# Kernel tuning notes

Measured on AMD Instinct MI355X. Metric: run time of the kernel, lower is better.

Reference implementation:

```python
import jax, jax.numpy as jnp
import numpy as np

N, E, G, F = 50000, 800000, 128, 64  # nodes, edges, graphs, feature dim
EPS = 1e-5


def setup_inputs() -> dict:
    key = jax.random.key(0)
    ks = jax.random.split(key, 16)
    w = lambda k, s: jax.random.normal(k, s, jnp.float32) * 0.05
    inp = {
        "x": jax.random.normal(ks[0], (N, F), jnp.float32),
        # SAGEConv l: lin_l (aggregated neighbors, with bias), lin_r (root, no bias)
        "c0_Wl": w(ks[1], (F, F)), "c0_bl": jnp.zeros((F,), jnp.float32), "c0_Wr": w(ks[2], (F, F)),
        "c1_Wl": w(ks[3], (F, F)), "c1_bl": jnp.zeros((F,), jnp.float32), "c1_Wr": w(ks[4], (F, F)),
        "c2_Wl": w(ks[5], (F, F)), "c2_bl": jnp.zeros((F,), jnp.float32), "c2_Wr": w(ks[6], (F, F)),
        # skip linears (bias=False)
        "s0_W": w(ks[7], (F, F)), "s1_W": w(ks[8], (F, F)),
        # graph-mode LayerNorm affine params
        "ln0_w": jnp.ones((F,), jnp.float32), "ln0_b": jnp.zeros((F,), jnp.float32),
        "ln1_w": jnp.ones((F,), jnp.float32), "ln1_b": jnp.zeros((F,), jnp.float32),
        "ln2_w": jnp.ones((F,), jnp.float32), "ln2_b": jnp.zeros((F,), jnp.float32),
        # PReLU(1): single shared slope, torch default init 0.25
        "p0_a": jnp.full((1,), 0.25, jnp.float32),
        "p1_a": jnp.full((1,), 0.25, jnp.float32),
        "p2_a": jnp.full((1,), 0.25, jnp.float32),
        "edge_index": jax.random.randint(ks[9], (2, E), 0, N, jnp.int64),
        "batch": jnp.sort(jax.random.randint(ks[10], (N,), 0, G, jnp.int64)),
    }
    return inp


def _sage(x, Wl, bl, Wr, src, dst):
    # mean-aggregate source features at destinations, then two linears
    agg = jax.ops.segment_sum(x[src], dst, num_segments=N)            # [N, F]
    deg = jax.ops.segment_sum(jnp.ones((E,), x.dtype), dst, num_segments=N)
    agg = agg / jnp.maximum(deg, 1.0)[:, None]
    return agg @ Wl + bl + x @ Wr


def _graph_ln(x, batch, w, b):
    # PyG LayerNorm mode='graph': normalize over all nodes & channels per graph
    f = x.shape[-1]
    cnt = jax.ops.segment_sum(jnp.ones((x.shape[0],), x.dtype), batch, num_segments=G)
    norm = jnp.maximum(cnt, 1.0) * f                                  # [G]
    mean = jax.ops.segment_sum(x, batch, num_segments=G).sum(-1) / norm
    xc = x - mean[batch][:, None]
    var = jax.ops.segment_sum(xc * xc, batch, num_segments=G).sum(-1) / norm
    out = xc / jnp.sqrt(var + EPS)[batch][:, None]
    return out * w + b


def _prelu(x, a):
    return jnp.where(x >= 0, x, a[0] * x)


def reference(x, c0_Wl, c0_bl, c0_Wr, c1_Wl, c1_bl, c1_Wr, c2_Wl, c2_bl, c2_Wr,
              s0_W, s1_W, ln0_w, ln0_b, ln1_w, ln1_b, ln2_w, ln2_b,
              p0_a, p1_a, p2_a, edge_index, batch):
    src, dst = edge_index[0], edge_index[1]
    h1 = _prelu(_graph_ln(_sage(x, c0_Wl, c0_bl, c0_Wr, src, dst), batch, ln0_w, ln0_b), p0_a)
    h2 = _sage(h1 + x @ s0_W, c1_Wl, c1_bl, c1_Wr, src, dst)
    h2 = _prelu(_graph_ln(h2, batch, ln1_w, ln1_b), p1_a)
    ret = _sage(h1 + h2 + x @ s1_W, c2_Wl, c2_bl, c2_Wr, src, dst)
    ret = _prelu(_graph_ln(ret, batch, ln2_w, ln2_b), p2_a)
    return ret
```

## Files before the change

kernel.cpp:

```cpp
#include <hip/hip_runtime.h>

#define NN 50000
#define NE 800000
#define NG 128
#define NF 64
#define EPSV 1e-5f
#define GB3 782
#define NBUCK 196
#define BCAP 5120

typedef unsigned short ushortT;

__device__ inline unsigned short f2bf(float f) {
  unsigned u = __float_as_uint(f);
  u += 0x7FFF + ((u >> 16) & 1);
  return (unsigned short)(u >> 16);
}
__device__ inline float bflo(unsigned v) { return __uint_as_float(v << 16); }
__device__ inline float bfhi(unsigned v) { return __uint_as_float(v & 0xFFFF0000u); }

__global__ void k_bz(const int* __restrict__ batch, int* __restrict__ bound,
                     int* __restrict__ gcursor, float* __restrict__ stats) {
  int i = blockIdx.x * 256 + threadIdx.x;
  if (blockIdx.x == 0) {
    int t = threadIdx.x;
    if (t < NBUCK) gcursor[t] = 0;
    for (int k = t; k < 6 * NG; k += 256) stats[k] = 0.f;
  }
  if (i >= NN) return;
  int b1 = batch[i];
  int b0 = (i == 0) ? -1 : batch[i - 1];
  for (int g = b0 + 1; g <= b1; ++g) bound[g] = i;
  if (i == NN - 1) {
    for (int g = b1 + 1; g <= NG; ++g) bound[g] = NN;
  }
}

__global__ __launch_bounds__(256) void k_cvt(const float* __restrict__ in,
                                             ushortT* __restrict__ outb) {
  int t = blockIdx.x * 256 + threadIdx.x;
  if (t >= NN * NF / 4) return;
  float4 v = ((const float4*)in)[t];
  ushort4 o;
  o.x = f2bf(v.x); o.y = f2bf(v.y); o.z = f2bf(v.z); o.w = f2bf(v.w);
  ((ushort4*)outb)[t] = o;
}

__global__ __launch_bounds__(256) void k_binA(const int* __restrict__ src,
                                              const int* __restrict__ dst,
                                              int* __restrict__ gcursor,
                                              int2* __restrict__ bbuf) {
  __shared__ int cnt[NBUCK], base[NBUCK], rank[NBUCK];
  int tid = threadIdx.x;
  if (tid < NBUCK) { cnt[tid] = 0; rank[tid] = 0; }
  __syncthreads();
  int e0 = blockIdx.x * 4096;
  int sv[16], dv[16], bk[16];
#pragma unroll
  for (int i = 0; i < 16; ++i) {
    int e = e0 + i * 256 + tid;
    if (e < NE) {
      sv[i] = src[e];
      dv[i] = dst[e];
      bk[i] = dv[i] >> 8;
      atomicAdd(&cnt[bk[i]], 1);
    } else bk[i] = -1;
  }
  __syncthreads();
  if (tid < NBUCK && cnt[tid] > 0) base[tid] = atomicAdd(&gcursor[tid], cnt[tid]);
  __syncthreads();
#pragma unroll
  for (int i = 0; i < 16; ++i) {
    if (bk[i] >= 0) {
      int p = base[bk[i]] + atomicAdd(&rank[bk[i]], 1);
      if (p < BCAP) bbuf[(size_t)bk[i] * BCAP + p] = make_int2(sv[i], dv[i]);
    }
  }
}

__global__ __launch_bounds__(256) void k_bscan(const int* __restrict__ gcursor,
                                               int* __restrict__ bbase,
                                               int* __restrict__ off) {
  __shared__ int sh[256];
  int tid = threadIdx.x;
  int v = (tid < NBUCK) ? gcursor[tid] : 0;
  sh[tid] = v;
  __syncthreads();
  for (int d = 1; d < 256; d <<= 1) {
    int t = (tid >= d) ? sh[tid - d] : 0;
    __syncthreads();
    sh[tid] += t;
    __syncthreads();
  }
  if (tid < NBUCK) bbase[tid] = sh[tid] - v;
  if (tid == NBUCK - 1) { bbase[NBUCK] = sh[tid]; off[NN] = sh[tid]; }
}

__global__ __launch_bounds__(256) void k_binB(const int2* __restrict__ bbuf,
                                              const int* __restrict__ gcursor,
                                              const int* __restrict__ bbase,
                                              int* __restrict__ off,
                                              int* __restrict__ csr) {
  __shared__ int cnt[256], cur[256], sh[256];
  int tid = threadIdx.x;
  int b = blockIdx.x;
  int nb = gcursor[b]; if (nb > BCAP) nb = BCAP;
  int gbase = bbase[b];
  cnt[tid] = 0;
  __syncthreads();
  const int2* bp = bbuf + (size_t)b * BCAP;
  for (int i = tid; i < nb; i += 256) {
    atomicAdd(&cnt[bp[i].y & 255], 1);
  }
  __syncthreads();
  int v = cnt[tid];
  sh[tid] = v;
  __syncthreads();
  for (int d = 1; d < 256; d <<= 1) {
    int t = (tid >= d) ? sh[tid - d] : 0;
    __syncthreads();
    sh[tid] += t;
    __syncthreads();
  }
  int excl = sh[tid] - v;
  cur[tid] = excl;
  int node = b * 256 + tid;
  if (node < NN) off[node] = gbase + excl;
  __syncthreads();
  for (int i = tid; i < nb; i += 256) {
    int2 e = bp[i];
    int p = atomicAdd(&cur[e.y & 255], 1);
    csr[gbase + p] = e.x;
  }
}

__global__ __launch_bounds__(256) void k_agg(const ushortT* __restrict__ in,
                                             const int* __restrict__ off,
                                             const int* __restrict__ csr,
                                             ushortT* __restrict__ out) {
  int t = blockIdx.x * 256 + threadIdx.x;
  int node = t >> 6;
  int lane = threadIdx.x & 63;
  int eo = lane >> 3;
  int fl = (lane & 7) << 3;
  if (node >= NN) return;
  int s0 = off[node], s1 = off[node + 1];
  float a0 = 0.f, a1 = 0.f, a2 = 0.f, a3 = 0.f, a4 = 0.f, a5 = 0.f, a6 = 0.f, a7 = 0.f;
  for (int j = s0 + eo; j < s1; j += 8) {
    int s = csr[j];
    uint4 v = *(const uint4*)&in[(size_t)s * NF + fl];
    a0 += bflo(v.x); a1 += bfhi(v.x);
    a2 += bflo(v.y); a3 += bfhi(v.y);
    a4 += bflo(v.z); a5 += bfhi(v.z);
    a6 += bflo(v.w); a7 += bfhi(v.w);
  }
#pragma unroll
  for (int d = 8; d < 64; d <<= 1) {
    a0 += __shfl_xor(a0, d); a1 += __shfl_xor(a1, d);
    a2 += __shfl_xor(a2, d); a3 += __shfl_xor(a3, d);
    a4 += __shfl_xor(a4, d); a5 += __shfl_xor(a5, d);
    a6 += __shfl_xor(a6, d); a7 += __shfl_xor(a7, d);
  }
  if (eo == 0) {
    int dg = s1 - s0;
    float inv = (dg > 0) ? 1.f / (float)dg : 0.f;
    uint4 o;
    o.x = (unsigned)f2bf(a0 * inv) | ((unsigned)f2bf(a1 * inv) << 16);
    o.y = (unsigned)f2bf(a2 * inv) | ((unsigned)f2bf(a3 * inv) << 16);
    o.z = (unsigned)f2bf(a4 * inv) | ((unsigned)f2bf(a5 * inv) << 16);
    o.w = (unsigned)f2bf(a6 * inv) | ((unsigned)f2bf(a7 * inv) << 16);
    *(uint4*)&out[(size_t)node * NF + fl] = o;
  }
}

__global__ __launch_bounds__(256) void k_sage_linear(const ushortT* __restrict__ A,
                                                     const ushortT* __restrict__ X,
                                                     const float* __restrict__ Wl,
                                                     const float* __restrict__ bl,
                                                     const float* __restrict__ Wr,
                                                     const int* __restrict__ batch,
                                                     float* __restrict__ gsum,
                                                     float* __restrict__ gsq,
                                                     float* __restrict__ out) {
  __shared__ float sh_s[4][64];
  __shared__ float sh_q[4][64];
  __shared__ float gs[NG];
  __shared__ float gq[NG];
  int tid = threadIdx.x;
  int lane = tid & 63;
  int wv = __builtin_amdgcn_readfirstlane(tid >> 6);
  int c0 = wv * 16;
  int row = blockIdx.x * 64 + lane;
  bool valid = row < NN;
  if (tid < NG) { gs[tid] = 0.f; gq[tid] = 0.f; }

  float acc[16];
#pragma unroll
  for (int cc = 0; cc < 16; ++cc) acc[cc] = bl[c0 + cc];

  int rsafe = valid ? row : 0;
  const ushortT* Ar = A + (size_t)rsafe * NF;
  const ushortT* Xr = X + (size_t)rsafe * NF;

  for (int k8 = 0; k8 < 8; ++k8) {
    uint4 av = *(const uint4*)&Ar[k8 * 8];
    float a0 = bflo(av.x), a1 = bfhi(av.x), a2 = bflo(av.y), a3 = bfhi(av.y);
    float a4 = bflo(av.z), a5 = bfhi(av.z), a6 = bflo(av.w), a7 = bfhi(av.w);
    const float* W0 = Wl + ((k8 * 8 + 0) * NF + c0);
    const float* W1 = Wl + ((k8 * 8 + 1) * NF + c0);
    const float* W2 = Wl + ((k8 * 8 + 2) * NF + c0);
    const float* W3 = Wl + ((k8 * 8 + 3) * NF + c0);
    const float* W4 = Wl + ((k8 * 8 + 4) * NF + c0);
    const float* W5 = Wl + ((k8 * 8 + 5) * NF + c0);
    const float* W6 = Wl + ((k8 * 8 + 6) * NF + c0);
    const float* W7 = Wl + ((k8 * 8 + 7) * NF + c0);
#pragma unroll
    for (int cc = 0; cc < 16; ++cc)
      acc[cc] += a0 * W0[cc] + a1 * W1[cc] + a2 * W2[cc] + a3 * W3[cc]
               + a4 * W4[cc] + a5 * W5[cc] + a6 * W6[cc] + a7 * W7[cc];
  }
  for (int k8 = 0; k8 < 8; ++k8) {
    uint4 xv = *(const uint4*)&Xr[k8 * 8];
    float a0 = bflo(xv.x), a1 = bfhi(xv.x), a2 = bflo(xv.y), a3 = bfhi(xv.y);
    float a4 = bflo(xv.z), a5 = bfhi(xv.z), a6 = bflo(xv.w), a7 = bfhi(xv.w);
    const float* W0 = Wr + ((k8 * 8 + 0) * NF + c0);
    const float* W1 = Wr + ((k8 * 8 + 1) * NF + c0);
    const float* W2 = Wr + ((k8 * 8 + 2) * NF + c0);
    const float* W3 = Wr + ((k8 * 8 + 3) * NF + c0);
    const float* W4 = Wr + ((k8 * 8 + 4) * NF + c0);
    const float* W5 = Wr + ((k8 * 8 + 5) * NF + c0);
    const float* W6 = Wr + ((k8 * 8 + 6) * NF + c0);
    const float* W7 = Wr + ((k8 * 8 + 7) * NF + c0);
#pragma unroll
    for (int cc = 0; cc < 16; ++cc)
      acc[cc] += a0 * W0[cc] + a1 * W1[cc] + a2 * W2[cc] + a3 * W3[cc]
               + a4 * W4[cc] + a5 * W5[cc] + a6 * W6[cc] + a7 * W7[cc];
  }

  if (valid) {
    float4* op = (float4*)(out + (size_t)row * NF + c0);
    op[0] = make_float4(acc[0], acc[1], acc[2], acc[3]);
    op[1] = make_float4(acc[4], acc[5], acc[6], acc[7]);
    op[2] = make_float4(acc[8], acc[9], acc[10], acc[11]);
    op[3] = make_float4(acc[12], acc[13], acc[14], acc[15]);
  }

  float s = 0.f, q = 0.f;
#pragma unroll
  for (int cc = 0; cc < 16; ++cc) { s += acc[cc]; q += acc[cc] * acc[cc]; }
  sh_s[wv][lane] = s;
  sh_q[wv][lane] = q;
  __syncthreads();
  if (tid < 64) {
    float ss = sh_s[0][lane] + sh_s[1][lane] + sh_s[2][lane] + sh_s[3][lane];
    float qq = sh_q[0][lane] + sh_q[1][lane] + sh_q[2][lane] + sh_q[3][lane];
    int r = blockIdx.x * 64 + lane;
    if (r < NN) {
      int g = batch[r];
      atomicAdd(&gs[g], ss);
      atomicAdd(&gq[g], qq);
    }
  }
  __syncthreads();
  if (tid < NG) {
    float fs = gs[tid], fq = gq[tid];
    if (fs != 0.f || fq != 0.f) { atomicAdd(&gsum[tid], fs); atomicAdd(&gsq[tid], fq); }
  }
}

__global__ __launch_bounds__(256) void k_skip_linear(
    const ushortT* __restrict__ X, const float* __restrict__ W,
    const float* __restrict__ t0, const float* __restrict__ gsum0, const float* __restrict__ gsq0,
    const float* __restrict__ lw0, const float* __restrict__ lb0, const float* __restrict__ pa0,
    const float* __restrict__ t1, const float* __restrict__ gsum1, const float* __restrict__ gsq1,
    const float* __restrict__ lw1, const float* __restrict__ lb1, const float* __restrict__ pa1,
    const int* __restrict__ batch, const int* __restrict__ bound,
    ushortT* __restrict__ outb) {
  int tid = threadIdx.x;
  int lane = tid & 63;
  int wv = __builtin_amdgcn_readfirstlane(tid >> 6);
  int c0 = wv * 16;
  int row = blockIdx.x * 64 + lane;
  bool valid = row < NN;
  int rsafe = valid ? row : 0;

  float acc[16];
#pragma unroll
  for (int cc = 0; cc < 16; ++cc) acc[cc] = 0.f;

  const ushortT* Xr = X + (size_t)rsafe * NF;
  for (int k8 = 0; k8 < 8; ++k8) {
    uint4 xv = *(const uint4*)&Xr[k8 * 8];
    float a0 = bflo(xv.x), a1 = bfhi(xv.x), a2 = bflo(xv.y), a3 = bfhi(xv.y);
    float a4 = bflo(xv.z), a5 = bfhi(xv.z), a6 = bflo(xv.w), a7 = bfhi(xv.w);
    const float* W0 = W + ((k8 * 8 + 0) * NF + c0);
    const float* W1 = W + ((k8 * 8 + 1) * NF + c0);
    const float* W2 = W + ((k8 * 8 + 2) * NF + c0);
    const float* W3 = W + ((k8 * 8 + 3) * NF + c0);
    const float* W4 = W + ((k8 * 8 + 4) * NF + c0);
    const float* W5 = W + ((k8 * 8 + 5) * NF + c0);
    const float* W6 = W + ((k8 * 8 + 6) * NF + c0);
    const float* W7 = W + ((k8 * 8 + 7) * NF + c0);
#pragma unroll
    for (int cc = 0; cc < 16; ++cc)
      acc[cc] += a0 * W0[cc] + a1 * W1[cc] + a2 * W2[cc] + a3 * W3[cc]
               + a4 * W4[cc] + a5 * W5[cc] + a6 * W6[cc] + a7 * W7[cc];
  }

  int g = batch[rsafe];
  float cntf = (float)(bound[g + 1] - bound[g]);
  float norm = fmaxf(cntf, 1.f) * (float)NF;
  {
    float m0 = gsum0[g] / norm;
    float v0 = gsq0[g] / norm - m0 * m0;
    float rs0 = rsqrtf(v0 + EPSV);
    float a0 = pa0[0];
    const float4* T0 = (const float4*)(t0 + (size_t)rsafe * NF + c0);
#pragma unroll
    for (int j = 0; j < 4; ++j) {
      float4 tv = T0[j];
      float tvv[4] = {tv.x, tv.y, tv.z, tv.w};
#pragma unroll
      for (int jj = 0; jj < 4; ++jj) {
        int cc = j * 4 + jj;
        float u = (tvv[jj] - m0) * rs0 * lw0[c0 + cc] + lb0[c0 + cc];
        acc[cc] += (u >= 0.f) ? u : a0 * u;
      }
    }
  }
  if (t1) {
    float m1 = gsum1[g] / norm;
    float v1 = gsq1[g] / norm - m1 * m1;
    float rs1 = rsqrtf(v1 + EPSV);
    float a1 = pa1[0];
    const float4* T1 = (const float4*)(t1 + (size_t)rsafe * NF + c0);
#pragma unroll
    for (int j = 0; j < 4; ++j) {
      float4 tv = T1[j];
      float tvv[4] = {tv.x, tv.y, tv.z, tv.w};
#pragma unroll
      for (int jj = 0; jj < 4; ++jj) {
        int cc = j * 4 + jj;
        float u = (tvv[jj] - m1) * rs1 * lw1[c0 + cc] + lb1[c0 + cc];
        acc[cc] += (u >= 0.f) ? u : a1 * u;
      }
    }
  }

  if (valid) {
    uint4 b0, b1v;
    b0.x = (unsigned)f2bf(acc[0]) | ((unsigned)f2bf(acc[1]) << 16);
    b0.y = (unsigned)f2bf(acc[2]) | ((unsigned)f2bf(acc[3]) << 16);
    b0.z = (unsigned)f2bf(acc[4]) | ((unsigned)f2bf(acc[5]) << 16);
    b0.w = (unsigned)f2bf(acc[6]) | ((unsigned)f2bf(acc[7]) << 16);
    b1v.x = (unsigned)f2bf(acc[8]) | ((unsigned)f2bf(acc[9]) << 16);
    b1v.y = (unsigned)f2bf(acc[10]) | ((unsigned)f2bf(acc[11]) << 16);
    b1v.z = (unsigned)f2bf(acc[12]) | ((unsigned)f2bf(acc[13]) << 16);
    b1v.w = (unsigned)f2bf(acc[14]) | ((unsigned)f2bf(acc[15]) << 16);
    uint4* obp = (uint4*)&outb[(size_t)row * NF + c0];
    obp[0] = b0;
    obp[1] = b1v;
  }
}

__global__ __launch_bounds__(256) void k_ln_apply(const float* __restrict__ t,
                                                  const int* __restrict__ batch,
                                                  const int* __restrict__ bound,
                                                  const float* __restrict__ gsum,
                                                  const float* __restrict__ gsq,
                                                  const float* __restrict__ w,
                                                  const float* __restrict__ b,
                                                  const float* __restrict__ alpha,
                                                  float* __restrict__ out) {
  int wid = (blockIdx.x * 256 + threadIdx.x) >> 6;
  int lane = threadIdx.x & 63;
  if (wid >= NN) return;
  int g = batch[wid];
  float cnt = (float)(bound[g + 1] - bound[g]);
  float norm = fmaxf(cnt, 1.f) * (float)NF;
  float mean = gsum[g] / norm;
  float var = gsq[g] / norm - mean * mean;
  float rstd = rsqrtf(var + EPSV);
  float a = alpha[0];
  float v = t[wid * NF + lane];
  v = (v - mean) * rstd;
  v = v * w[lane] + b[lane];
  out[wid * NF + lane] = (v >= 0.f) ? v : a * v;
}

extern "C" void kernel_launch(void* const* d_in, const int* in_sizes, int n_in,
                              void* d_out, int out_size, void* d_ws, size_t ws_size,
                              hipStream_t stream) {
  const float* x     = (const float*)d_in[0];
  const float* c0_Wl = (const float*)d_in[1];
  const float* c0_bl = (const float*)d_in[2];
  const float* c0_Wr = (const float*)d_in[3];
  const float* c1_Wl = (const float*)d_in[4];
  const float* c1_bl = (const float*)d_in[5];
  const float* c1_Wr = (const float*)d_in[6];
  const float* c2_Wl = (const float*)d_in[7];
  const float* c2_bl = (const float*)d_in[8];
  const float* c2_Wr = (const float*)d_in[9];
  const float* s0_W  = (const float*)d_in[10];
  const float* s1_W  = (const float*)d_in[11];
  const float* ln0_w = (const float*)d_in[12];
  const float* ln0_b = (const float*)d_in[13];
  const float* ln1_w = (const float*)d_in[14];
  const float* ln1_b = (const float*)d_in[15];
  const float* ln2_w = (const float*)d_in[16];
  const float* ln2_b = (const float*)d_in[17];
  const float* p0_a  = (const float*)d_in[18];
  const float* p1_a  = (const float*)d_in[19];
  const float* p2_a  = (const float*)d_in[20];
  const int*   ei    = (const int*)d_in[21];
  const int*   batch = (const int*)d_in[22];
  float* out = (float*)d_out;

  const int* src = ei;
  const int* dst = ei + NE;

  char* ws = (char*)d_ws;
  const size_t off_gcur   = 0;
  const size_t off_stats  = 200704;
  const size_t off_bound  = 204800;
  const size_t off_off    = 205824;
  const size_t off_bbase  = 406272;
  const size_t off_csr    = 607744;
  const size_t off_B1     = 3807744;
  const size_t off_B2     = off_B1 + 12800000;
  const size_t off_B4     = off_B2 + 12800000;
  const size_t off_xb     = off_B4 + 12800000;
  const size_t off_B3b    = off_xb + 6400000;

  int*    gcursor = (int*)(ws + off_gcur);
  float*  stats   = (float*)(ws + off_stats);
  int*    bound   = (int*)(ws + off_bound);
  int*    offp    = (int*)(ws + off_off);
  int*    bbase   = (int*)(ws + off_bbase);
  int*    csr     = (int*)(ws + off_csr);
  int2*   bbuf    = (int2*)(ws + off_B1);
  ushortT* B1b    = (ushortT*)(ws + off_B1);
  float*  B2      = (float*)(ws + off_B2);
  float*  B4      = (float*)(ws + off_B4);
  ushortT* xb     = (ushortT*)(ws + off_xb);
  ushortT* B3b    = (ushortT*)(ws + off_B3b);
  (void)ws_size; (void)in_sizes; (void)n_in; (void)out_size;

  float* gsum0 = stats + 0 * NG; float* gsq0 = stats + 1 * NG;
  float* gsum1 = stats + 2 * NG; float* gsq1 = stats + 3 * NG;
  float* gsum2 = stats + 4 * NG; float* gsq2 = stats + 5 * NG;

  const int NB  = (NN + 255) / 256;
  const int WB  = (NN * 64 + 255) / 256;
  const int CB  = (NN * NF / 4 + 255) / 256;

  k_bz<<<NB, 256, 0, stream>>>(batch, bound, gcursor, stats);
  k_cvt<<<CB, 256, 0, stream>>>(x, xb);
  k_binA<<<NBUCK, 256, 0, stream>>>(src, dst, gcursor, bbuf);
  k_bscan<<<1, 256, 0, stream>>>(gcursor, bbase, offp);
  k_binB<<<NBUCK, 256, 0, stream>>>(bbuf, gcursor, bbase, offp, csr);

  k_agg<<<WB, 256, 0, stream>>>(xb, offp, csr, B1b);
  k_sage_linear<<<GB3, 256, 0, stream>>>(B1b, xb, c0_Wl, c0_bl, c0_Wr, batch, gsum0, gsq0, B2);
  k_skip_linear<<<GB3, 256, 0, stream>>>(xb, s0_W,
                                         B2, gsum0, gsq0, ln0_w, ln0_b, p0_a,
                                         nullptr, nullptr, nullptr, nullptr, nullptr, nullptr,
                                         batch, bound, B3b);

  k_agg<<<WB, 256, 0, stream>>>(B3b, offp, csr, B1b);
  k_sage_linear<<<GB3, 256, 0, stream>>>(B1b, B3b, c1_Wl, c1_bl, c1_Wr, batch, gsum1, gsq1, B4);
  k_skip_linear<<<GB3, 256, 0, stream>>>(xb, s1_W,
                                         B2, gsum0, gsq0, ln0_w, ln0_b, p0_a,
                                         B4, gsum1, gsq1, ln1_w, ln1_b, p1_a,
                                         batch, bound, B3b);

  k_agg<<<WB, 256, 0, stream>>>(B3b, offp, csr, B1b);
  k_sage_linear<<<GB3, 256, 0, stream>>>(B1b, B3b, c2_Wl, c2_bl, c2_Wr, batch, gsum2, gsq2, out);
  k_ln_apply<<<WB, 256, 0, stream>>>(out, batch, bound, gsum2, gsq2, ln2_w, ln2_b, p2_a, out);
}
```

Baseline: 211.9 us.

## Fuse preprocessing kernels, drop bucket scan, store intermediates in bf16, precompute skip

Merges the batch-boundary and fp32-to-bf16 conversion kernels into one launch. It removes the bucket scan kernel by giving each bucket a fixed BCAP-sized slot and packing offset and degree into one int per node. Intermediate SAGE outputs are now stored as bf16 instead of fp32, which halves their traffic. Both skip linears are computed in the first skip kernel, so the second skip step becomes a purely elementwise kernel. The CSR becomes sparse with gaps, and the extra bf16 rounding slightly reduces accuracy.

```diff
diff --git a/kernel.cpp b/kernel.cpp
--- a/kernel.cpp
+++ b/kernel.cpp
@@ -8,6 +8,7 @@
 #define GB3 782
 #define NBUCK 196
 #define BCAP 5120
+#define OFFMASK 0xFFFFF
 
 typedef unsigned short ushortT;
 
@@ -19,31 +20,35 @@
 __device__ inline float bflo(unsigned v) { return __uint_as_float(v << 16); }
 __device__ inline float bfhi(unsigned v) { return __uint_as_float(v & 0xFFFF0000u); }
 
-__global__ void k_bz(const int* __restrict__ batch, int* __restrict__ bound,
-                     int* __restrict__ gcursor, float* __restrict__ stats) {
-  int i = blockIdx.x * 256 + threadIdx.x;
+__global__ __launch_bounds__(256) void k_pre(const float* __restrict__ x,
+                                             ushortT* __restrict__ xb,
+                                             const int* __restrict__ batch,
+                                             int* __restrict__ bound,
+                                             int* __restrict__ gcursor,
+                                             float* __restrict__ stats) {
+  int t = blockIdx.x * 256 + threadIdx.x;
+  if (t < NN * NF / 4) {
+    float4 v = ((const float4*)x)[t];
+    ushort4 o;
+    o.x = f2bf(v.x); o.y = f2bf(v.y); o.z = f2bf(v.z); o.w = f2bf(v.w);
+    ((ushort4*)xb)[t] = o;
+  }
   if (blockIdx.x == 0) {
-    int t = threadIdx.x;
-    if (t < NBUCK) gcursor[t] = 0;
-    for (int k = t; k < 6 * NG; k += 256) stats[k] = 0.f;
-  }
-  if (i >= NN) return;
-  int b1 = batch[i];
-  int b0 = (i == 0) ? -1 : batch[i - 1];
-  for (int g = b0 + 1; g <= b1; ++g) bound[g] = i;
-  if (i == NN - 1) {
-    for (int g = b1 + 1; g <= NG; ++g) bound[g] = NN;
-  }
-}
-
-__global__ __launch_bounds__(256) void k_cvt(const float* __restrict__ in,
-                                             ushortT* __restrict__ outb) {
-  int t = blockIdx.x * 256 + threadIdx.x;
-  if (t >= NN * NF / 4) return;
-  float4 v = ((const float4*)in)[t];
-  ushort4 o;
-  o.x = f2bf(v.x); o.y = f2bf(v.y); o.z = f2bf(v.z); o.w = f2bf(v.w);
-  ((ushort4*)outb)[t] = o;
+    int tt = threadIdx.x;
+    if (tt < NBUCK) gcursor[tt] = 0;
+    for (int k = tt; k < 6 * NG; k += 256) stats[k] = 0.f;
+  }
+  if (blockIdx.x < (NN + 255) / 256) {
+    int i = blockIdx.x * 256 + threadIdx.x;
+    if (i < NN) {
+      int b1 = batch[i];
+      int b0 = (i == 0) ? -1 : batch[i - 1];
+      for (int g = b0 + 1; g <= b1; ++g) bound[g] = i;
+      if (i == NN - 1) {
+        for (int g = b1 + 1; g <= NG; ++g) bound[g] = NN;
+      }
+    }
+  }
 }
 
 __global__ __launch_bounds__(256) void k_binA(const int* __restrict__ src,
@@ -67,23 +72,35 @@
     } else bk[i] = -1;
   }
   __syncthreads();
-  if (tid < NBUCK && cnt[tid] > 0) base[tid] = atomicAdd(&gcursor[tid], cnt[tid]);
+  if (tid < NBUCK && cnt[tid] > 0)
+    base[tid] = tid * BCAP + atomicAdd(&gcursor[tid], cnt[tid]);
   __syncthreads();
 #pragma unroll
   for (int i = 0; i < 16; ++i) {
     if (bk[i] >= 0) {
       int p = base[bk[i]] + atomicAdd(&rank[bk[i]], 1);
-      if (p < BCAP) bbuf[(size_t)bk[i] * BCAP + p] = make_int2(sv[i], dv[i]);
+      if (p < (bk[i] + 1) * BCAP) bbuf[p] = make_int2(sv[i], dv[i]);
     }
   }
 }
 
-__global__ __launch_bounds__(256) void k_bscan(const int* __restrict__ gcursor,
-                                               int* __restrict__ bbase,
-                                               int* __restrict__ off) {
-  __shared__ int sh[256];
+__global__ __launch_bounds__(256) void k_binB(const int2* __restrict__ bbuf,
+                                              const int* __restrict__ gcursor,
+                                              int* __restrict__ offdeg,
+                                              int* __restrict__ csr) {
+  __shared__ int cnt[256], cur[256], sh[256];
   int tid = threadIdx.x;
-  int v = (tid < NBUCK) ? gcursor[tid] : 0;
+  int b = blockIdx.x;
+  int nb = gcursor[b]; if (nb > BCAP) nb = BCAP;
+  int gbase = b * BCAP;
+  cnt[tid] = 0;
+  __syncthreads();
+  const int2* bp = bbuf + (size_t)gbase;
+  for (int i = tid; i < nb; i += 256) {
+    atomicAdd(&cnt[bp[i].y & 255], 1);
+  }
+  __syncthreads();
+  int v = cnt[tid];
   sh[tid] = v;
   __syncthreads();
   for (int d = 1; d < 256; d <<= 1) {
@@ -92,40 +109,10 @@
     sh[tid] += t;
     __syncthreads();
   }
-  if (tid < NBUCK) bbase[tid] = sh[tid] - v;
-  if (tid == NBUCK - 1) { bbase[NBUCK] = sh[tid]; off[NN] = sh[tid]; }
-}
-
-__global__ __launch_bounds__(256) void k_binB(const int2* __restrict__ bbuf,
-                                              const int* __restrict__ gcursor,
-                                              const int* __restrict__ bbase,
-                                              int* __restrict__ off,
-                                              int* __restrict__ csr) {
-  __shared__ int cnt[256], cur[256], sh[256];
-  int tid = threadIdx.x;
-  int b = blockIdx.x;
-  int nb = gcursor[b]; if (nb > BCAP) nb = BCAP;
-  int gbase = bbase[b];
-  cnt[tid] = 0;
-  __syncthreads();
-  const int2* bp = bbuf + (size_t)b * BCAP;
-  for (int i = tid; i < nb; i += 256) {
-    atomicAdd(&cnt[bp[i].y & 255], 1);
-  }
-  __syncthreads();
-  int v = cnt[tid];
-  sh[tid] = v;
-  __syncthreads();
-  for (int d = 1; d < 256; d <<= 1) {
-    int t = (tid >= d) ? sh[tid - d] : 0;
-    __syncthreads();
-    sh[tid] += t;
-    __syncthreads();
-  }
   int excl = sh[tid] - v;
   cur[tid] = excl;
   int node = b * 256 + tid;
-  if (node < NN) off[node] = gbase + excl;
+  if (node < NN) offdeg[node] = (gbase + excl) | (v << 20);
   __syncthreads();
   for (int i = tid; i < nb; i += 256) {
     int2 e = bp[i];
@@ -135,7 +122,7 @@
 }
 
 __global__ __launch_bounds__(256) void k_agg(const ushortT* __restrict__ in,
-                                             const int* __restrict__ off,
+                                             const int* __restrict__ offdeg,
                                              const int* __restrict__ csr,
                                              ushortT* __restrict__ out) {
   int t = blockIdx.x * 256 + threadIdx.x;
@@ -144,7 +131,10 @@
   int eo = lane >> 3;
   int fl = (lane & 7) << 3;
   if (node >= NN) return;
-  int s0 = off[node], s1 = off[node + 1];
+  int od = offdeg[node];
+  int s0 = od & OFFMASK;
+  int dg = od >> 20;
+  int s1 = s0 + dg;
   float a0 = 0.f, a1 = 0.f, a2 = 0.f, a3 = 0.f, a4 = 0.f, a5 = 0.f, a6 = 0.f, a7 = 0.f;
   for (int j = s0 + eo; j < s1; j += 8) {
     int s = csr[j];
@@ -162,7 +152,6 @@
     a6 += __shfl_xor(a6, d); a7 += __shfl_xor(a7, d);
   }
   if (eo == 0) {
-    int dg = s1 - s0;
     float inv = (dg > 0) ? 1.f / (float)dg : 0.f;
     uint4 o;
     o.x = (unsigned)f2bf(a0 * inv) | ((unsigned)f2bf(a1 * inv) << 16);
@@ -181,7 +170,8 @@
                                                      const int* __restrict__ batch,
                                                      float* __restrict__ gsum,
                                                      float* __restrict__ gsq,
-                                                     float* __restrict__ out) {
+                                                     float* __restrict__ outf,
+                                                     ushortT* __restrict__ outb) {
   __shared__ float sh_s[4][64];
   __shared__ float sh_q[4][64];
   __shared__ float gs[NG];
@@ -238,11 +228,26 @@
   }
 
   if (valid) {
-    float4* op = (float4*)(out + (size_t)row * NF + c0);
-    op[0] = make_float4(acc[0], acc[1], acc[2], acc[3]);
-    op[1] = make_float4(acc[4], acc[5], acc[6], acc[7]);
-    op[2] = make_float4(acc[8], acc[9], acc[10], acc[11]);
-    op[3] = make_float4(acc[12], acc[13], acc[14], acc[15]);
+    if (outf) {
+      float4* op = (float4*)(outf + (size_t)row * NF + c0);
+      op[0] = make_float4(acc[0], acc[1], acc[2], acc[3]);
+      op[1] = make_float4(acc[4], acc[5], acc[6], acc[7]);
+      op[2] = make_float4(acc[8], acc[9], acc[10], acc[11]);
+      op[3] = make_float4(acc[12], acc[13], acc[14], acc[15]);
+    } else {
+      uint4 b0, b1v;
+      b0.x = (unsigned)f2bf(acc[0]) | ((unsigned)f2bf(acc[1]) << 16);
+      b0.y = (unsigned)f2bf(acc[2]) | ((unsigned)f2bf(acc[3]) << 16);
+      b0.z = (unsigned)f2bf(acc[4]) | ((unsigned)f2bf(acc[5]) << 16);
+      b0.w = (unsigned)f2bf(acc[6]) | ((unsigned)f2bf(acc[7]) << 16);
+      b1v.x = (unsigned)f2bf(acc[8]) | ((unsigned)f2bf(acc[9]) << 16);
+      b1v.y = (unsigned)f2bf(acc[10]) | ((unsigned)f2bf(acc[11]) << 16);
+      b1v.z = (unsigned)f2bf(acc[12]) | ((unsigned)f2bf(acc[13]) << 16);
+      b1v.w = (unsigned)f2bf(acc[14]) | ((unsigned)f2bf(acc[15]) << 16);
+      uint4* obp = (uint4*)&outb[(size_t)row * NF + c0];
+      obp[0] = b0;
+      obp[1] = b1v;
+    }
   }
 
   float s = 0.f, q = 0.f;
@@ -268,14 +273,14 @@
   }
 }
 
-__global__ __launch_bounds__(256) void k_skip_linear(
-    const ushortT* __restrict__ X, const float* __restrict__ W,
-    const float* __restrict__ t0, const float* __restrict__ gsum0, const float* __restrict__ gsq0,
+__global__ __launch_bounds__(256) void k_skip0(
+    const ushortT* __restrict__ X,
+    const float* __restrict__ W0p, const float* __restrict__ W1p,
+    const ushortT* __restrict__ t0b,
+    const float* __restrict__ gsum0, const float* __restrict__ gsq0,
     const float* __restrict__ lw0, const float* __restrict__ lb0, const float* __restrict__ pa0,
-    const float* __restrict__ t1, const float* __restrict__ gsum1, const float* __restrict__ gsq1,
-    const float* __restrict__ lw1, const float* __restrict__ lb1, const float* __restrict__ pa1,
     const int* __restrict__ batch, const int* __restrict__ bound,
-    ushortT* __restrict__ outb) {
+    ushortT* __restrict__ z1b, ushortT* __restrict__ xs1b) {
   int tid = threadIdx.x;
   int lane = tid & 63;
   int wv = __builtin_amdgcn_readfirstlane(tid >> 6);
@@ -284,83 +289,134 @@
   bool valid = row < NN;
   int rsafe = valid ? row : 0;
 
-  float acc[16];
-#pragma unroll
-  for (int cc = 0; cc < 16; ++cc) acc[cc] = 0.f;
+  float acc0[16], acc1[16];
+#pragma unroll
+  for (int cc = 0; cc < 16; ++cc) { acc0[cc] = 0.f; acc1[cc] = 0.f; }
 
   const ushortT* Xr = X + (size_t)rsafe * NF;
   for (int k8 = 0; k8 < 8; ++k8) {
     uint4 xv = *(const uint4*)&Xr[k8 * 8];
     float a0 = bflo(xv.x), a1 = bfhi(xv.x), a2 = bflo(xv.y), a3 = bfhi(xv.y);
     float a4 = bflo(xv.z), a5 = bfhi(xv.z), a6 = bflo(xv.w), a7 = bfhi(xv.w);
-    const float* W0 = W + ((k8 * 8 + 0) * NF + c0);
-    const float* W1 = W + ((k8 * 8 + 1) * NF + c0);
-    const float* W2 = W + ((k8 * 8 + 2) * NF + c0);
-    const float* W3 = W + ((k8 * 8 + 3) * NF + c0);
-    const float* W4 = W + ((k8 * 8 + 4) * NF + c0);
-    const float* W5 = W + ((k8 * 8 + 5) * NF + c0);
-    const float* W6 = W + ((k8 * 8 + 6) * NF + c0);
-    const float* W7 = W + ((k8 * 8 + 7) * NF + c0);
-#pragma unroll
-    for (int cc = 0; cc < 16; ++cc)
-      acc[cc] += a0 * W0[cc] + a1 * W1[cc] + a2 * W2[cc] + a3 * W3[cc]
-               + a4 * W4[cc] + a5 * W5[cc] + a6 * W6[cc] + a7 * W7[cc];
+    const float* P0 = W0p + ((k8 * 8 + 0) * NF + c0);
+    const float* P1 = W0p + ((k8 * 8 + 1) * NF + c0);
+    const float* P2 = W0p + ((k8 * 8 + 2) * NF + c0);
+    const float* P3 = W0p + ((k8 * 8 + 3) * NF + c0);
+    const float* P4 = W0p + ((k8 * 8 + 4) * NF + c0);
+    const float* P5 = W0p + ((k8 * 8 + 5) * NF + c0);
+    const float* P6 = W0p + ((k8 * 8 + 6) * NF + c0);
+    const float* P7 = W0p + ((k8 * 8 + 7) * NF + c0);
+    const float* Q0 = W1p + ((k8 * 8 + 0) * NF + c0);
+    const float* Q1 = W1p + ((k8 * 8 + 1) * NF + c0);
+    const float* Q2 = W1p + ((k8 * 8 + 2) * NF + c0);
+    const float* Q3 = W1p + ((k8 * 8 + 3) * NF + c0);
+    const float* Q4 = W1p + ((k8 * 8 + 4) * NF + c0);
+    const float* Q5 = W1p + ((k8 * 8 + 5) * NF + c0);
+    const float* Q6 = W1p + ((k8 * 8 + 6) * NF + c0);
+    const float* Q7 = W1p + ((k8 * 8 + 7) * NF + c0);
+#pragma unroll
+    for (int cc = 0; cc < 16; ++cc) {
+      acc0[cc] += a0 * P0[cc] + a1 * P1[cc] + a2 * P2[cc] + a3 * P3[cc]
+                + a4 * P4[cc] + a5 * P5[cc] + a6 * P6[cc] + a7 * P7[cc];
+      acc1[cc] += a0 * Q0[cc] + a1 * Q1[cc] + a2 * Q2[cc] + a3 * Q3[cc]
+                + a4 * Q4[cc] + a5 * Q5[cc] + a6 * Q6[cc] + a7 * Q7[cc];
+    }
   }
 
   int g = batch[rsafe];
   float cntf = (float)(bound[g + 1] - bound[g]);
   float norm = fmaxf(cntf, 1.f) * (float)NF;
-  {
-    float m0 = gsum0[g] / norm;
-    float v0 = gsq0[g] / norm - m0 * m0;
-    float rs0 = rsqrtf(v0 + EPSV);
-    float a0 = pa0[0];
-    const float4* T0 = (const float4*)(t0 + (size_t)rsafe * NF + c0);
-#pragma unroll
-    for (int j = 0; j < 4; ++j) {
-      float4 tv = T0[j];
-      float tvv[4] = {tv.x, tv.y, tv.z, tv.w};
-#pragma unroll
-      for (int jj = 0; jj < 4; ++jj) {
-        int cc = j * 4 + jj;
-        float u = (tvv[jj] - m0) * rs0 * lw0[c0 + cc] + lb0[c0 + cc];
-        acc[cc] += (u >= 0.f) ? u : a0 * u;
-      }
+  float m0 = gsum0[g] / norm;
+  float v0 = gsq0[g] / norm - m0 * m0;
+  float rs0 = rsqrtf(v0 + EPSV);
+  float a0p = pa0[0];
+  const uint4* T0 = (const uint4*)(t0b + (size_t)rsafe * NF + c0);
+#pragma unroll
+  for (int j = 0; j < 2; ++j) {
+    uint4 tv = T0[j];
+    float tvv[8] = {bflo(tv.x), bfhi(tv.x), bflo(tv.y), bfhi(tv.y),
+                    bflo(tv.z), bfhi(tv.z), bflo(tv.w), bfhi(tv.w)};
+#pragma unroll
+    for (int jj = 0; jj < 8; ++jj) {
+      int cc = j * 8 + jj;
+      float u = (tvv[jj] - m0) * rs0 * lw0[c0 + cc] + lb0[c0 + cc];
+      acc0[cc] += (u >= 0.f) ? u : a0p * u;
     }
   }
-  if (t1) {
-    float m1 = gsum1[g] / norm;
-    float v1 = gsq1[g] / norm - m1 * m1;
-    float rs1 = rsqrtf(v1 + EPSV);
-    float a1 = pa1[0];
-    const float4* T1 = (const float4*)(t1 + (size_t)rsafe * NF + c0);
-#pragma unroll
-    for (int j = 0; j < 4; ++j) {
-      float4 tv = T1[j];
-      float tvv[4] = {tv.x, tv.y, tv.z, tv.w};
-#pragma unroll
-      for (int jj = 0; jj < 4; ++jj) {
-        int cc = j * 4 + jj;
-        float u = (tvv[jj] - m1) * rs1 * lw1[c0 + cc] + lb1[c0 + cc];
-        acc[cc] += (u >= 0.f) ? u : a1 * u;
-      }
-    }
-  }
 
   if (valid) {
-    uint4 b0, b1v;
-    b0.x = (unsigned)f2bf(acc[0]) | ((unsigned)f2bf(acc[1]) << 16);
-    b0.y = (unsigned)f2bf(acc[2]) | ((unsigned)f2bf(acc[3]) << 16);
-    b0.z = (unsigned)f2bf(acc[4]) | ((unsigned)f2bf(acc[5]) << 16);
-    b0.w = (unsigned)f2bf(acc[6]) | ((unsigned)f2bf(acc[7]) << 16);
-    b1v.x = (unsigned)f2bf(acc[8]) | ((unsigned)f2bf(acc[9]) << 16);
-    b1v.y = (unsigned)f2bf(acc[10]) | ((unsigned)f2bf(acc[11]) << 16);
-    b1v.z = (unsigned)f2bf(acc[12]) | ((unsigned)f2bf(acc[13]) << 16);
-    b1v.w = (unsigned)f2bf(acc[14]) | ((unsigned)f2bf(acc[15]) << 16);
-    uint4* obp = (uint4*)&outb[(size_t)row * NF + c0];
-    obp[0] = b0;
-    obp[1] = b1v;
-  }
+    uint4 o0, o1;
+    o0.x = (unsigned)f2bf(acc0[0]) | ((unsigned)f2bf(acc0[1]) << 16);
+    o0.y = (unsigned)f2bf(acc0[2]) | ((unsigned)f2bf(acc0[3]) << 16);
+    o0.z = (unsigned)f2bf(acc0[4]) | ((unsigned)f2bf(acc0[5]) << 16);
+    o0.w = (unsigned)f2bf(acc0[6]) | ((unsigned)f2bf(acc0[7]) << 16);
+    o1.x = (unsigned)f2bf(acc0[8]) | ((unsigned)f2bf(acc0[9]) << 16);
+    o1.y = (unsigned)f2bf(acc0[10]) | ((unsigned)f2bf(acc0[11]) << 16);
+    o1.z = (unsigned)f2bf(acc0[12]) | ((unsigned)f2bf(acc0[13]) << 16);
+    o1.w = (unsigned)f2bf(acc0[14]) | ((unsigned)f2bf(acc0[15]) << 16);
+    uint4* zp = (uint4*)&z1b[(size_t)row * NF + c0];
+    zp[0] = o0; zp[1] = o1;
+    uint4 s0v, s1v;
+    s0v.x = (unsigned)f2bf(acc1[0]) | ((unsigned)f2bf(acc1[1]) << 16);
+    s0v.y = (unsigned)f2bf(acc1[2]) | ((unsigned)f2bf(acc1[3]) << 16);
+    s0v.z = (unsigned)f2bf(acc1[4]) | ((unsigned)f2bf(acc1[5]) << 16);
+    s0v.w = (unsigned)f2bf(acc1[6]) | ((unsigned)f2bf(acc1[7]) << 16);
+    s1v.x = (unsigned)f2bf(acc1[8]) | ((unsigned)f2bf(acc1[9]) << 16);
+    s1v.y = (unsigned)f2bf(acc1[10]) | ((unsigned)f2bf(acc1[11]) << 16);
+    s1v.z = (unsigned)f2bf(acc1[12]) | ((unsigned)f2bf(acc1[13]) << 16);
+    s1v.w = (unsigned)f2bf(acc1[14]) | ((unsigned)f2bf(acc1[15]) << 16);
+    uint4* sp = (uint4*)&xs1b[(size_t)row * NF + c0];
+    sp[0] = s0v; sp[1] = s1v;
+  }
+}
+
+__global__ __launch_bounds__(256) void k_skip1(
+    const ushortT* __restrict__ h1b, const ushortT* __restrict__ h2b,
+    const ushortT* __restrict__ xs1b,
+    const float* __restrict__ gsum0, const float* __restrict__ gsq0,
+    const float* __restrict__ lw0, const float* __restrict__ lb0, const float* __restrict__ pa0,
+    const float* __restrict__ gsum1, const float* __restrict__ gsq1,
+    const float* __restrict__ lw1, const float* __restrict__ lb1, const float* __restrict__ pa1,
+    const int* __restrict__ batch, const int* __restrict__ bound,
+    ushortT* __restrict__ z2b) {
+  int t = blockIdx.x * 256 + threadIdx.x;
+  if (t >= NN * NF / 8) return;
+  int row = t >> 3;
+  int f0 = (t & 7) * 8;
+  int g = batch[row];
+  float cntf = (float)(bound[g + 1] - bound[g]);
+  float norm = fmaxf(cntf, 1.f) * (float)NF;
+  float m0 = gsum0[g] / norm;
+  float va0 = gsq0[g] / norm - m0 * m0;
+  float rs0 = rsqrtf(va0 + EPSV);
+  float m1 = gsum1[g] / norm;
+  float va1 = gsq1[g] / norm - m1 * m1;
+  float rs1 = rsqrtf(va1 + EPSV);
+  float a0 = pa0[0], a1 = pa1[0];
+  uint4 h1 = ((const uint4*)h1b)[t];
+  uint4 h2 = ((const uint4*)h2b)[t];
+  uint4 xs = ((const uint4*)xs1b)[t];
+  float r[8];
+  float h1v[8] = {bflo(h1.x), bfhi(h1.x), bflo(h1.y), bfhi(h1.y),
+                  bflo(h1.z), bfhi(h1.z), bflo(h1.w), bfhi(h1.w)};
+  float h2v[8] = {bflo(h2.x), bfhi(h2.x), bflo(h2.y), bfhi(h2.y),
+                  bflo(h2.z), bfhi(h2.z), bflo(h2.w), bfhi(h2.w)};
+  float xsv[8] = {bflo(xs.x), bfhi(xs.x), bflo(xs.y), bfhi(xs.y),
+                  bflo(xs.z), bfhi(xs.z), bflo(xs.w), bfhi(xs.w)};
+#pragma unroll
+  for (int j = 0; j < 8; ++j) {
+    float u = (h1v[j] - m0) * rs0 * lw0[f0 + j] + lb0[f0 + j];
+    u = (u >= 0.f) ? u : a0 * u;
+    float w = (h2v[j] - m1) * rs1 * lw1[f0 + j] + lb1[f0 + j];
+    w = (w >= 0.f) ? w : a1 * w;
+    r[j] = u + w + xsv[j];
+  }
+  uint4 o;
+  o.x = (unsigned)f2bf(r[0]) | ((unsigned)f2bf(r[1]) << 16);
+  o.y = (unsigned)f2bf(r[2]) | ((unsigned)f2bf(r[3]) << 16);
+  o.z = (unsigned)f2bf(r[4]) | ((unsigned)f2bf(r[5]) << 16);
+  o.w = (unsigned)f2bf(r[6]) | ((unsigned)f2bf(r[7]) << 16);
+  ((uint4*)z2b)[t] = o;
 }
 
 __global__ __launch_bounds__(256) void k_ln_apply(const float* __restrict__ t,
@@ -421,60 +477,61 @@
 
   char* ws = (char*)d_ws;
   const size_t off_gcur   = 0;
-  const size_t off_stats  = 200704;
-  const size_t off_bound  = 204800;
-  const size_t off_off    = 205824;
-  const size_t off_bbase  = 406272;
-  const size_t off_csr    = 607744;
-  const size_t off_B1     = 3807744;
-  const size_t off_B2     = off_B1 + 12800000;
-  const size_t off_B4     = off_B2 + 12800000;
-  const size_t off_xb     = off_B4 + 12800000;
+  const size_t off_stats  = 4096;
+  const size_t off_bound  = 8192;
+  const size_t off_od     = 12288;
+  const size_t off_csr    = 262144;
+  const size_t off_bbuf   = 4980736;
+  const size_t off_B1b    = off_bbuf;
+  const size_t off_B2b    = 13631488;
+  const size_t off_B4b    = off_B2b + 6400000;
+  const size_t off_xb     = off_B4b + 6400000;
   const size_t off_B3b    = off_xb + 6400000;
+  const size_t off_xs1b   = off_B3b + 6400000;
 
   int*    gcursor = (int*)(ws + off_gcur);
   float*  stats   = (float*)(ws + off_stats);
   int*    bound   = (int*)(ws + off_bound);
-  int*    offp    = (int*)(ws + off_off);
-  int*    bbase   = (int*)(ws + off_bbase);
+  int*    offdeg  = (int*)(ws + off_od);
   int*    csr     = (int*)(ws + off_csr);
-  int2*   bbuf    = (int2*)(ws + off_B1);
-  ushortT* B1b    = (ushortT*)(ws + off_B1);
-  float*  B2      = (float*)(ws + off_B2);
-  float*  B4      = (float*)(ws + off_B4);
+  int2*   bbuf    = (int2*)(ws + off_bbuf);
+  ushortT* B1b    = (ushortT*)(ws + off_B1b);
+  ushortT* B2b    = (ushortT*)(ws + off_B2b);
+  ushortT* B4b    = (ushortT*)(ws + off_B4b);
   ushortT* xb     = (ushortT*)(ws + off_xb);
   ushortT* B3b    = (ushortT*)(ws + off_B3b);
+  ushortT* xs1b   = (ushortT*)(ws + off_xs1b);
   (void)ws_size; (void)in_sizes; (void)n_in; (void)out_size;
 
   float* gsum0 = stats + 0 * NG; float* gsq0 = stats + 1 * NG;
   float* gsum1 = stats + 2 * NG; float* gsq1 = stats + 3 * NG;
   float* gsum2 = stats + 4 * NG; float* gsq2 = stats + 5 * NG;
 
-  const int NB  = (NN + 255) / 256;
   const int WB  = (NN * 64 + 255) / 256;
   const int CB  = (NN * NF / 4 + 255) / 256;
-
-  k_bz<<<NB, 256, 0, stream>>>(batch, bound, gcursor, stats);
-  k_cvt<<<CB, 256, 0, stream>>>(x, xb);
+  const int EWB = (NN * NF / 8 + 255) / 256;
+
+  k_pre<<<CB, 256, 0, stream>>>(x, xb, batch, bound, gcursor, stats);
   k_binA<<<NBUCK, 256, 0, stream>>>(src, dst, gcursor, bbuf);
-  k_bscan<<<1, 256, 0, stream>>>(gcursor, bbase, offp);
-  k_binB<<<NBUCK, 256, 0, stream>>>(bbuf, gcursor, bbase, offp, csr);
-
-  k_agg<<<WB, 256, 0, stream>>>(xb, offp, csr, B1b);
-  k_sage_linear<<<GB3, 256, 0, stream>>>(B1b, xb, c0_Wl, c0_bl, c0_Wr, batch, gsum0, gsq0, B2);
-  k_skip_linear<<<GB3, 256, 0, stream>>>(xb, s0_W,
-                                         B2, gsum0, gsq0, ln0_w, ln0_b, p0_a,
-                                         nullptr, nullptr, nullptr, nullptr, nullptr, nullptr,
-                                         batch, bound, B3b);
-
-  k_agg<<<WB, 256, 0, stream>>>(B3b, offp, csr, B1b);
-  k_sage_linear<<<GB3, 256, 0, stream>>>(B1b, B3b, c1_Wl, c1_bl, c1_Wr, batch, gsum1, gsq1, B4);
-  k_skip_linear<<<GB3, 256, 0, stream>>>(xb, s1_W,
-                                         B2, gsum0, gsq0, ln0_w, ln0_b, p0_a,
-                                         B4, gsum1, gsq1, ln1_w, ln1_b, p1_a,
-                                         batch, bound, B3b);
-
-  k_agg<<<WB, 256, 0, stream>>>(B3b, offp, csr, B1b);
-  k_sage_linear<<<GB3, 256, 0, stream>>>(B1b, B3b, c2_Wl, c2_bl, c2_Wr, batch, gsum2, gsq2, out);
+  k_binB<<<NBUCK, 256, 0, stream>>>(bbuf, gcursor, offdeg, csr);
+
+  k_agg<<<WB, 256, 0, stream>>>(xb, offdeg, csr, B1b);
+  k_sage_linear<<<GB3, 256, 0, stream>>>(B1b, xb, c0_Wl, c0_bl, c0_Wr,
+                                         batch, gsum0, gsq0, nullptr, B2b);
+  k_skip0<<<GB3, 256, 0, stream>>>(xb, s0_W, s1_W,
+                                   B2b, gsum0, gsq0, ln0_w, ln0_b, p0_a,
+                                   batch, bound, B3b, xs1b);
+
+  k_agg<<<WB, 256, 0, stream>>>(B3b, offdeg, csr, B1b);
+  k_sage_linear<<<GB3, 256, 0, stream>>>(B1b, B3b, c1_Wl, c1_bl, c1_Wr,
+                                         batch, gsum1, gsq1, nullptr, B4b);
+  k_skip1<<<EWB, 256, 0, stream>>>(B2b, B4b, xs1b,
+                                   gsum0, gsq0, ln0_w, ln0_b, p0_a,
+                                   gsum1, gsq1, ln1_w, ln1_b, p1_a,
+                                   batch, bound, B3b);
+
+  k_agg<<<WB, 256, 0, stream>>>(B3b, offdeg, csr, B1b);
+  k_sage_linear<<<GB3, 256, 0, stream>>>(B1b, B3b, c2_Wl, c2_bl, c2_Wr,
+                                         batch, gsum2, gsq2, out, nullptr);
   k_ln_apply<<<WB, 256, 0, stream>>>(out, batch, bound, gsum2, gsq2, ln2_w, ln2_b, p2_a, out);
 }
```

New measurement: 210.6 us. No clear change (-0.6%).
